# Performance work log

Hardware: AMD Instinct MI355X
Metric: run time of the kernel (lower is better)

Reference implementation:

```python
import jax, jax.numpy as jnp
import numpy as np

B, T = 256, 2048
K_LABELS = 50
K2 = K_LABELS + 2  # includes START (K) and STOP (K+1) tags
NEG_INF = -10000.0


def setup_inputs() -> dict:
    key = jax.random.key(0)
    k1, k2, k3, k4 = jax.random.split(key, 4)
    emissions = jax.random.normal(k1, (B, T, K2), dtype=jnp.float32)
    transitions = jax.random.normal(k2, (K2, K2), dtype=jnp.float32)
    lengths = jax.random.randint(k3, (B,), 1, T + 1, dtype=jnp.int64)
    labels = jax.random.randint(k4, (B, T), 0, K_LABELS, dtype=jnp.int64)
    return {"emissions": emissions, "transitions": transitions,
            "lengths": lengths, "labels": labels}


def _forward_algo(emissions, transitions, lengths):
    b, t, k2 = emissions.shape
    start_tag, stop_tag = k2 - 2, k2 - 1
    init = jnp.full((k2,), NEG_INF, emissions.dtype).at[start_tag].set(0.0)
    alpha0 = jnp.broadcast_to(init, (b, k2))  # [B, K2]

    def step(alpha, emit):
        # tag_var[b, next, prev] = emit[b, next] + trans[next, prev] + alpha[b, prev]
        tag_var = emit[:, :, None] + transitions[None, :, :] + alpha[:, None, :]
        new_alpha = jax.nn.logsumexp(tag_var, axis=2)  # [B, K2]
        return new_alpha, new_alpha

    _, alphas = jax.lax.scan(step, alpha0, jnp.swapaxes(emissions, 0, 1))
    all_alphas = jnp.concatenate([alpha0[None], alphas], axis=0)  # [T+1, B, K2]
    fv = all_alphas[lengths, jnp.arange(b)]  # alpha at each sequence's final step
    terminal = fv + transitions[stop_tag][None, :]
    return jax.nn.logsumexp(terminal, axis=1)  # [B]


def _score_label(emissions, transitions, lengths, labels):
    b, t, k2 = emissions.shape
    start_tag, stop_tag = k2 - 2, k2 - 1
    start_col = jnp.full((b, 1), start_tag, labels.dtype)
    stop_col = jnp.full((b, 1), stop_tag, labels.dtype)
    pad_start = jnp.concatenate([start_col, labels], axis=1)  # [B, T+1]
    pad_stop = jnp.concatenate([labels, stop_col], axis=1)    # [B, T+1]
    pos = jnp.arange(t + 1)
    pad_stop = jnp.where(pos[None, :] >= lengths[:, None], stop_tag, pad_stop)
    # transition score over positions 0..length (inclusive)
    trans_mask = pos[None, :] <= lengths[:, None]
    trans_sc = jnp.where(trans_mask, transitions[pad_stop, pad_start], 0.0).sum(axis=1)
    # emission score over positions 0..length-1
    emit_mask = jnp.arange(t)[None, :] < lengths[:, None]
    emit_vals = jnp.take_along_axis(emissions, labels[..., None], axis=-1)[..., 0]
    emit_sc = jnp.where(emit_mask, emit_vals, 0.0).sum(axis=1)
    return trans_sc + emit_sc  # [B]


def reference(emissions, transitions, lengths, labels):
    forward_score = _forward_algo(emissions, transitions, lengths)
    gold_score = _score_label(emissions, transitions, lengths, labels)
    return jnp.mean(forward_score - gold_score)
```

## Files before the change

### kernel.cpp

```cpp
#include <hip/hip_runtime.h>


#define B_    256
#define T_    2048
#define K2_   52
#define LOG2E_ 1.4426950408889634f
#define LN2_   0.6931471805599453f

__device__ __forceinline__ int imin(int a, int b) { return a < b ? a : b; }
__device__ __forceinline__ int imax(int a, int b) { return a > b ? a : b; }

#define FORALL52(F) \
  F(0) F(1) F(2) F(3) F(4) F(5) F(6) F(7) F(8) F(9) F(10) F(11) F(12) F(13) \
  F(14) F(15) F(16) F(17) F(18) F(19) F(20) F(21) F(22) F(23) F(24) F(25) \
  F(26) F(27) F(28) F(29) F(30) F(31) F(32) F(33) F(34) F(35) F(36) F(37) \
  F(38) F(39) F(40) F(41) F(42) F(43) F(44) F(45) F(46) F(47) F(48) F(49) \
  F(50) F(51)

#define DECLM_F(i) float M_##i; { float _t = tr[n * K2_ + i] * LOG2E_; \
  asm("v_exp_f32 %0, %1\n\ts_nop 1" : "=v"(M_##i) : "v"(_t)); }
#define DECLM_B(i) float M_##i; { float _t = tr[i * K2_ + n] * LOG2E_; \
  asm("v_exp_f32 %0, %1\n\ts_nop 1" : "=v"(M_##i) : "v"(_t)); }

#define ACCQ(Q, i0,i1,i2,i3) \
  _a0 = fmaf(M_##i0, (Q).x, _a0); \
  _a1 = fmaf(M_##i1, (Q).y, _a1); \
  _a2 = fmaf(M_##i2, (Q).z, _a2); \
  _a3 = fmaf(M_##i3, (Q).w, _a3);

#define ACC_ALL \
  ACCQ(_q0 , 0, 1, 2, 3)  ACCQ(_q1 , 4, 5, 6, 7)  ACCQ(_q2 , 8, 9,10,11) \
  ACCQ(_q3 ,12,13,14,15)  ACCQ(_q4 ,16,17,18,19)  ACCQ(_q5 ,20,21,22,23) \
  ACCQ(_q6 ,24,25,26,27)  ACCQ(_q7 ,28,29,30,31)  ACCQ(_q8 ,32,33,34,35) \
  ACCQ(_q9 ,36,37,38,39)  ACCQ(_q10,40,41,42,43)  ACCQ(_q11,44,45,46,47) \
  ACCQ(_qc ,48,49,50,51)

#define MATVEC_F(OUTY, RENORMV) \
    const float4* _g4 = (const float4*)sh; \
    float4 _qc  = _g4[12]; \
    float4 _q0  = _g4[0],  _q1  = _g4[1],  _q2  = _g4[2],  _q3  = _g4[3]; \
    float4 _q4  = _g4[4],  _q5  = _g4[5],  _q6  = _g4[6],  _q7  = _g4[7]; \
    float4 _q8  = _g4[8],  _q9  = _g4[9],  _q10 = _g4[10], _q11 = _g4[11]; \
    float RENORMV = _qc.z; (void)RENORMV; \
    float _a0 = 0.0f, _a1 = 0.0f, _a2 = 0.0f, _a3 = 0.0f; \
    ACC_ALL \
    float OUTY = (_a0 + _a1) + (_a2 + _a3);

#define MATVEC_B(OUTY, RENORMV) \
    const float4* _g4 = (const float4*)sh; \
    float4 _q0  = _g4[0]; \
    float4 _q1  = _g4[1],  _q2  = _g4[2],  _q3  = _g4[3],  _q4  = _g4[4]; \
    float4 _q5  = _g4[5],  _q6  = _g4[6],  _q7  = _g4[7],  _q8  = _g4[8]; \
    float4 _q9  = _g4[9],  _q10 = _g4[10], _q11 = _g4[11], _qc  = _g4[12]; \
    float RENORMV = _q0.x; (void)RENORMV; \
    float _a0 = 0.0f, _a1 = 0.0f, _a2 = 0.0f, _a3 = 0.0f; \
    ACC_ALL \
    float OUTY = (_a0 + _a1) + (_a2 + _a3);

#define FSTEP_R(EV, NEWIDX) do {                                \
    float _ne  = emb[(size_t)(NEWIDX) * K2_ + n];               \
    MATVEC_F(_y, _m)                                            \
    float _inv = __builtin_amdgcn_rcpf(_m);                     \
    C += __builtin_amdgcn_logf(_m);                             \
    float _E = __builtin_amdgcn_exp2f((EV) * LOG2E_);           \
    vv = _y * (_inv * _E);                                      \
    sh[lane] = vv;                                              \
    EV = _ne;                                                   \
  } while (0)
#define FSTEP_N(EV, NEWIDX) do {                                \
    float _ne  = emb[(size_t)(NEWIDX) * K2_ + n];               \
    MATVEC_F(_y, _mu)                                           \
    float _E = __builtin_amdgcn_exp2f((EV) * LOG2E_);           \
    vv = _y * _E;                                               \
    sh[lane] = vv;                                              \
    EV = _ne;                                                   \
  } while (0)

#define BSTEP_R(EV, NEWIDX) do {                                \
    float _ne  = emb[(size_t)(NEWIDX) * K2_ + n];               \
    MATVEC_B(_y, _m)                                            \
    float _inv = __builtin_amdgcn_rcpf(_m);                     \
    C += __builtin_amdgcn_logf(_m);                             \
    vv = _y * _inv;                                             \
    float _E = __builtin_amdgcn_exp2f((EV) * LOG2E_);           \
    sh[lane] = vv * _E;                                         \
    EV = _ne;                                                   \
  } while (0)
#define BSTEP_N(EV, NEWIDX) do {                                \
    float _ne  = emb[(size_t)(NEWIDX) * K2_ + n];               \
    MATVEC_B(_y, _mu)                                           \
    vv = _y;                                                    \
    float _E = __builtin_amdgcn_exp2f((EV) * LOG2E_);           \
    sh[lane] = vv * _E;                                         \
    EV = _ne;                                                   \
  } while (0)

__launch_bounds__(128, 1)
__global__ void crf_fwd_kernel(const float* __restrict__ em,
                               const float* __restrict__ tr,
                               const int*  __restrict__ len,
                               const int*  __restrict__ lab,
                               float* __restrict__ per_b)
{
  const int b    = blockIdx.x;
  const int tid  = threadIdx.x;
  const int wave = tid >> 6;
  const int lane = tid & 63;
  const int n    = (lane < K2_) ? lane : (K2_ - 1);
  const int L    = len[b];
  const int h    = L >> 1;
  const float* emb = em + (size_t)b * (T_ * K2_);

  __shared__ __align__(16) float sV[2][64];
  __shared__ float sCb[1];
  __shared__ float sG[2];

  float* sh = sV[wave];
  float vv, C = 0.0f;

  if (wave == 0) {
    FORALL52(DECLM_F)
    vv = (lane == 50) ? 1.0f : 0.0f;
    sh[lane] = vv;
    float e0 = emb[0 * K2_ + n];
    float e1 = emb[1 * K2_ + n];
    float e2 = emb[2 * K2_ + n];
    float e3 = emb[3 * K2_ + n];
    int t = 0;
    for (; t + 4 <= h; t += 4) {
      int i4 = imin(t + 4, T_ - 1), i5 = imin(t + 5, T_ - 1);
      int i6 = imin(t + 6, T_ - 1), i7 = imin(t + 7, T_ - 1);
      FSTEP_R(e0, i4);
      FSTEP_N(e1, i5);
      FSTEP_N(e2, i6);
      FSTEP_N(e3, i7);
    }
    int rem = h - t;
    if (rem > 0) FSTEP_R(e0, T_ - 1);
    if (rem > 1) FSTEP_N(e1, T_ - 1);
    if (rem > 2) FSTEP_N(e2, T_ - 1);
  } else {
    FORALL52(DECLM_B)
    vv = __builtin_amdgcn_exp2f(tr[(K2_ - 1) * K2_ + n] * LOG2E_);
    int cnt = L - h;
    float e0 = emb[(size_t)(L - 1) * K2_ + n];
    float eA = emb[(size_t)imax(L - 2, 0) * K2_ + n];
    float eB = emb[(size_t)imax(L - 3, 0) * K2_ + n];
    float eC = emb[(size_t)imax(L - 4, 0) * K2_ + n];
    float eD = emb[(size_t)imax(L - 5, 0) * K2_ + n];
    sh[lane] = vv * __builtin_amdgcn_exp2f(e0 * LOG2E_);
    int s = 0;
    for (; s + 4 <= cnt; s += 4) {
      int j4 = imax(L - 6 - s, 0), j5 = imax(L - 7 - s, 0);
      int j6 = imax(L - 8 - s, 0), j7 = imax(L - 9 - s, 0);
      BSTEP_R(eA, j4);
      BSTEP_N(eB, j5);
      BSTEP_N(eC, j6);
      BSTEP_N(eD, j7);
    }
    int rem = cnt - s;
    if (rem > 0) BSTEP_R(eA, 0);
    if (rem > 1) BSTEP_N(eB, 0);
    if (rem > 2) BSTEP_N(eC, 0);

    sh[lane] = vv;
    if (lane == 0) sCb[0] = C;
  }

  float gold = 0.0f;
  const int* labb = lab + b * T_;
  for (int tt = tid; tt < L; tt += 128) {
    int l1 = labb[tt];
    int l0 = (tt == 0) ? 50 : labb[tt - 1];
    gold += emb[(size_t)tt * K2_ + l1] + tr[l1 * K2_ + l0];
  }
  if (tid == 0) gold += tr[(K2_ - 1) * K2_ + labb[L - 1]];
#pragma unroll
  for (int off = 32; off >= 1; off >>= 1)
    gold += __shfl_xor(gold, off, 64);
  if (lane == 0) sG[wave] = gold;

  __syncthreads();

  if (wave == 0) {
    float x = (lane < K2_) ? vv * sV[1][lane] : 0.0f;
#pragma unroll
    for (int off = 32; off >= 1; off >>= 1)
      x += __shfl_xor(x, off, 64);
    float fwd = (C + sCb[0] + __builtin_amdgcn_logf(x)) * LN2_;
    if (lane == 0) per_b[b] = fwd - (sG[0] + sG[1]);
  }
}

__global__ void reduce_mean_kernel(const float* __restrict__ per_b,
                                   float* __restrict__ out)
{
  const int tid = threadIdx.x;
  float v = per_b[tid];
#pragma unroll
  for (int off = 32; off >= 1; off >>= 1) v += __shfl_xor(v, off, 64);
  __shared__ float s[4];
  if ((tid & 63) == 0) s[tid >> 6] = v;
  __syncthreads();
  if (tid == 0) out[0] = ((s[0] + s[1]) + (s[2] + s[3])) * (1.0f / (float)B_);
}

extern "C" void kernel_launch(void* const* d_in, const int* in_sizes, int n_in,
                              void* d_out, int out_size, void* d_ws, size_t ws_size,
                              hipStream_t stream) {
  const float* em  = (const float*)d_in[0];
  const float* tr  = (const float*)d_in[1];
  const int*   len = (const int*)d_in[2];
  const int*   lab = (const int*)d_in[3];
  float* out = (float*)d_out;
  float* ws  = (float*)d_ws;

  crf_fwd_kernel<<<B_, 128, 0, stream>>>(em, tr, len, lab, ws);
  reduce_mean_kernel<<<1, 256, 0, stream>>>(ws, out);
}
```

Baseline: 395.4 us.

## Interleave forward and backward recursions in a single wave per sequence

Instead of two waves each running one half-chain (forward alpha and backward beta), one 64-lane wave now holds both transition matrices in registers and interleaves forward and backward steps. The two independent dependency chains can hide each other's LDS and transcendental latency, and the block barrier and shared-memory merge go away. Shared-memory reads in the matvec are also split into two batches of eight float4 loads that reuse registers. In exchange each wave needs about 104 matrix registers plus temporaries, which raises register pressure and risks spills, and the 256 blocks now supply only 256 waves in total.

```diff
diff --git a/kernel.cpp b/kernel.cpp
--- a/kernel.cpp
+++ b/kernel.cpp
@@ -17,44 +17,62 @@
   F(38) F(39) F(40) F(41) F(42) F(43) F(44) F(45) F(46) F(47) F(48) F(49) \
   F(50) F(51)
 
-#define DECLM_F(i) float M_##i; { float _t = tr[n * K2_ + i] * LOG2E_; \
-  asm("v_exp_f32 %0, %1\n\ts_nop 1" : "=v"(M_##i) : "v"(_t)); }
-#define DECLM_B(i) float M_##i; { float _t = tr[i * K2_ + n] * LOG2E_; \
-  asm("v_exp_f32 %0, %1\n\ts_nop 1" : "=v"(M_##i) : "v"(_t)); }
-
-#define ACCQ(Q, i0,i1,i2,i3) \
-  _a0 = fmaf(M_##i0, (Q).x, _a0); \
-  _a1 = fmaf(M_##i1, (Q).y, _a1); \
-  _a2 = fmaf(M_##i2, (Q).z, _a2); \
-  _a3 = fmaf(M_##i3, (Q).w, _a3);
-
-#define ACC_ALL \
-  ACCQ(_q0 , 0, 1, 2, 3)  ACCQ(_q1 , 4, 5, 6, 7)  ACCQ(_q2 , 8, 9,10,11) \
-  ACCQ(_q3 ,12,13,14,15)  ACCQ(_q4 ,16,17,18,19)  ACCQ(_q5 ,20,21,22,23) \
-  ACCQ(_q6 ,24,25,26,27)  ACCQ(_q7 ,28,29,30,31)  ACCQ(_q8 ,32,33,34,35) \
-  ACCQ(_q9 ,36,37,38,39)  ACCQ(_q10,40,41,42,43)  ACCQ(_q11,44,45,46,47) \
-  ACCQ(_qc ,48,49,50,51)
+#define DECLMF(i) float MF_##i; { float _t = tr[n * K2_ + i] * LOG2E_; \
+  asm("v_exp_f32 %0, %1\n\ts_nop 1" : "=v"(MF_##i) : "v"(_t)); }
+#define DECLMB(i) float MB_##i; { float _t = tr[i * K2_ + n] * LOG2E_; \
+  asm("v_exp_f32 %0, %1\n\ts_nop 1" : "=v"(MB_##i) : "v"(_t)); }
+
+#define ACCQF(Q, i0,i1,i2,i3) \
+  _a0 = fmaf(MF_##i0, (Q).x, _a0); \
+  _a1 = fmaf(MF_##i1, (Q).y, _a1); \
+  _a2 = fmaf(MF_##i2, (Q).z, _a2); \
+  _a3 = fmaf(MF_##i3, (Q).w, _a3);
+#define ACCQB(Q, i0,i1,i2,i3) \
+  _a0 = fmaf(MB_##i0, (Q).x, _a0); \
+  _a1 = fmaf(MB_##i1, (Q).y, _a1); \
+  _a2 = fmaf(MB_##i2, (Q).z, _a2); \
+  _a3 = fmaf(MB_##i3, (Q).w, _a3);
 
 #define MATVEC_F(OUTY, RENORMV) \
-    const float4* _g4 = (const float4*)sh; \
-    float4 _qc  = _g4[12]; \
-    float4 _q0  = _g4[0],  _q1  = _g4[1],  _q2  = _g4[2],  _q3  = _g4[3]; \
-    float4 _q4  = _g4[4],  _q5  = _g4[5],  _q6  = _g4[6],  _q7  = _g4[7]; \
-    float4 _q8  = _g4[8],  _q9  = _g4[9],  _q10 = _g4[10], _q11 = _g4[11]; \
-    float RENORMV = _qc.z; (void)RENORMV; \
+    const float4* _g4 = (const float4*)sF; \
+    float4 _r0 = _g4[12], _r1 = _g4[0], _r2 = _g4[1], _r3 = _g4[2]; \
+    float4 _r4 = _g4[3],  _r5 = _g4[4], _r6 = _g4[5], _r7 = _g4[6]; \
+    float RENORMV = _r0.z; (void)RENORMV; \
     float _a0 = 0.0f, _a1 = 0.0f, _a2 = 0.0f, _a3 = 0.0f; \
-    ACC_ALL \
+    ACCQF(_r0,48,49,50,51)  _r0 = _g4[7]; \
+    ACCQF(_r1, 0, 1, 2, 3)  _r1 = _g4[8]; \
+    ACCQF(_r2, 4, 5, 6, 7)  _r2 = _g4[9]; \
+    ACCQF(_r3, 8, 9,10,11)  _r3 = _g4[10]; \
+    ACCQF(_r4,12,13,14,15)  _r4 = _g4[11]; \
+    ACCQF(_r5,16,17,18,19) \
+    ACCQF(_r6,20,21,22,23) \
+    ACCQF(_r7,24,25,26,27) \
+    ACCQF(_r0,28,29,30,31) \
+    ACCQF(_r1,32,33,34,35) \
+    ACCQF(_r2,36,37,38,39) \
+    ACCQF(_r3,40,41,42,43) \
+    ACCQF(_r4,44,45,46,47) \
     float OUTY = (_a0 + _a1) + (_a2 + _a3);
 
 #define MATVEC_B(OUTY, RENORMV) \
-    const float4* _g4 = (const float4*)sh; \
-    float4 _q0  = _g4[0]; \
-    float4 _q1  = _g4[1],  _q2  = _g4[2],  _q3  = _g4[3],  _q4  = _g4[4]; \
-    float4 _q5  = _g4[5],  _q6  = _g4[6],  _q7  = _g4[7],  _q8  = _g4[8]; \
-    float4 _q9  = _g4[9],  _q10 = _g4[10], _q11 = _g4[11], _qc  = _g4[12]; \
-    float RENORMV = _q0.x; (void)RENORMV; \
+    const float4* _g4 = (const float4*)sB; \
+    float4 _r0 = _g4[0], _r1 = _g4[1], _r2 = _g4[2], _r3 = _g4[3]; \
+    float4 _r4 = _g4[4], _r5 = _g4[5], _r6 = _g4[6], _r7 = _g4[7]; \
+    float RENORMV = _r0.x; (void)RENORMV; \
     float _a0 = 0.0f, _a1 = 0.0f, _a2 = 0.0f, _a3 = 0.0f; \
-    ACC_ALL \
+    ACCQB(_r0, 0, 1, 2, 3)  _r0 = _g4[8]; \
+    ACCQB(_r1, 4, 5, 6, 7)  _r1 = _g4[9]; \
+    ACCQB(_r2, 8, 9,10,11)  _r2 = _g4[10]; \
+    ACCQB(_r3,12,13,14,15)  _r3 = _g4[11]; \
+    ACCQB(_r4,16,17,18,19)  _r4 = _g4[12]; \
+    ACCQB(_r5,20,21,22,23) \
+    ACCQB(_r6,24,25,26,27) \
+    ACCQB(_r7,28,29,30,31) \
+    ACCQB(_r0,32,33,34,35) \
+    ACCQB(_r1,36,37,38,39) \
+    ACCQB(_r2,40,41,42,43) \
+    ACCQB(_r3,44,45,46,47) \
+    ACCQB(_r4,48,49,50,51) \
     float OUTY = (_a0 + _a1) + (_a2 + _a3);
 
 #define FSTEP_R(EV, NEWIDX) do {                                \
@@ -63,16 +81,16 @@
     float _inv = __builtin_amdgcn_rcpf(_m);                     \
     C += __builtin_amdgcn_logf(_m);                             \
     float _E = __builtin_amdgcn_exp2f((EV) * LOG2E_);           \
-    vv = _y * (_inv * _E);                                      \
-    sh[lane] = vv;                                              \
+    vf = _y * (_inv * _E);                                      \
+    sF[lane] = vf;                                              \
     EV = _ne;                                                   \
   } while (0)
 #define FSTEP_N(EV, NEWIDX) do {                                \
     float _ne  = emb[(size_t)(NEWIDX) * K2_ + n];               \
     MATVEC_F(_y, _mu)                                           \
     float _E = __builtin_amdgcn_exp2f((EV) * LOG2E_);           \
-    vv = _y * _E;                                               \
-    sh[lane] = vv;                                              \
+    vf = _y * _E;                                               \
+    sF[lane] = vf;                                              \
     EV = _ne;                                                   \
   } while (0)
 
@@ -81,21 +99,21 @@
     MATVEC_B(_y, _m)                                            \
     float _inv = __builtin_amdgcn_rcpf(_m);                     \
     C += __builtin_amdgcn_logf(_m);                             \
-    vv = _y * _inv;                                             \
-    float _E = __builtin_amdgcn_exp2f((EV) * LOG2E_);           \
-    sh[lane] = vv * _E;                                         \
+    vb = _y * _inv;                                             \
+    float _E = __builtin_amdgcn_exp2f((EV) * LOG2E_);           \
+    sB[lane] = vb * _E;                                         \
     EV = _ne;                                                   \
   } while (0)
 #define BSTEP_N(EV, NEWIDX) do {                                \
     float _ne  = emb[(size_t)(NEWIDX) * K2_ + n];               \
     MATVEC_B(_y, _mu)                                           \
-    vv = _y;                                                    \
-    float _E = __builtin_amdgcn_exp2f((EV) * LOG2E_);           \
-    sh[lane] = vv * _E;                                         \
-    EV = _ne;                                                   \
-  } while (0)
-
-__launch_bounds__(128, 1)
+    vb = _y;                                                    \
+    float _E = __builtin_amdgcn_exp2f((EV) * LOG2E_);           \
+    sB[lane] = vb * _E;                                         \
+    EV = _ne;                                                   \
+  } while (0)
+
+__launch_bounds__(64, 1)
 __global__ void crf_fwd_kernel(const float* __restrict__ em,
                                const float* __restrict__ tr,
                                const int*  __restrict__ len,
@@ -103,93 +121,76 @@
                                float* __restrict__ per_b)
 {
   const int b    = blockIdx.x;
-  const int tid  = threadIdx.x;
-  const int wave = tid >> 6;
-  const int lane = tid & 63;
+  const int lane = threadIdx.x & 63;
   const int n    = (lane < K2_) ? lane : (K2_ - 1);
   const int L    = len[b];
   const int h    = L >> 1;
+  const int cnt  = L - h;
   const float* emb = em + (size_t)b * (T_ * K2_);
 
-  __shared__ __align__(16) float sV[2][64];
-  __shared__ float sCb[1];
-  __shared__ float sG[2];
-
-  float* sh = sV[wave];
-  float vv, C = 0.0f;
-
-  if (wave == 0) {
-    FORALL52(DECLM_F)
-    vv = (lane == 50) ? 1.0f : 0.0f;
-    sh[lane] = vv;
-    float e0 = emb[0 * K2_ + n];
-    float e1 = emb[1 * K2_ + n];
-    float e2 = emb[2 * K2_ + n];
-    float e3 = emb[3 * K2_ + n];
-    int t = 0;
-    for (; t + 4 <= h; t += 4) {
-      int i4 = imin(t + 4, T_ - 1), i5 = imin(t + 5, T_ - 1);
-      int i6 = imin(t + 6, T_ - 1), i7 = imin(t + 7, T_ - 1);
-      FSTEP_R(e0, i4);
-      FSTEP_N(e1, i5);
-      FSTEP_N(e2, i6);
-      FSTEP_N(e3, i7);
-    }
-    int rem = h - t;
-    if (rem > 0) FSTEP_R(e0, T_ - 1);
-    if (rem > 1) FSTEP_N(e1, T_ - 1);
-    if (rem > 2) FSTEP_N(e2, T_ - 1);
-  } else {
-    FORALL52(DECLM_B)
-    vv = __builtin_amdgcn_exp2f(tr[(K2_ - 1) * K2_ + n] * LOG2E_);
-    int cnt = L - h;
-    float e0 = emb[(size_t)(L - 1) * K2_ + n];
-    float eA = emb[(size_t)imax(L - 2, 0) * K2_ + n];
-    float eB = emb[(size_t)imax(L - 3, 0) * K2_ + n];
-    float eC = emb[(size_t)imax(L - 4, 0) * K2_ + n];
-    float eD = emb[(size_t)imax(L - 5, 0) * K2_ + n];
-    sh[lane] = vv * __builtin_amdgcn_exp2f(e0 * LOG2E_);
-    int s = 0;
-    for (; s + 4 <= cnt; s += 4) {
-      int j4 = imax(L - 6 - s, 0), j5 = imax(L - 7 - s, 0);
-      int j6 = imax(L - 8 - s, 0), j7 = imax(L - 9 - s, 0);
-      BSTEP_R(eA, j4);
-      BSTEP_N(eB, j5);
-      BSTEP_N(eC, j6);
-      BSTEP_N(eD, j7);
-    }
-    int rem = cnt - s;
-    if (rem > 0) BSTEP_R(eA, 0);
-    if (rem > 1) BSTEP_N(eB, 0);
-    if (rem > 2) BSTEP_N(eC, 0);
-
-    sh[lane] = vv;
-    if (lane == 0) sCb[0] = C;
+  __shared__ __align__(16) float sF[64];
+  __shared__ __align__(16) float sB[64];
+
+  float C = 0.0f;
+
+  FORALL52(DECLMF)
+  FORALL52(DECLMB)
+
+  float vf = (lane == 50) ? 1.0f : 0.0f;
+  sF[lane] = vf;
+  float f0 = emb[0 * K2_ + n];
+  float f1 = emb[1 * K2_ + n];
+  float f2 = emb[2 * K2_ + n];
+  float f3 = emb[3 * K2_ + n];
+
+  float vb = __builtin_amdgcn_exp2f(tr[(K2_ - 1) * K2_ + n] * LOG2E_);
+  float e0 = emb[(size_t)(L - 1) * K2_ + n];
+  float bA = emb[(size_t)imax(L - 2, 0) * K2_ + n];
+  float bB = emb[(size_t)imax(L - 3, 0) * K2_ + n];
+  float bC = emb[(size_t)imax(L - 4, 0) * K2_ + n];
+  float bD = emb[(size_t)imax(L - 5, 0) * K2_ + n];
+  sB[lane] = vb * __builtin_amdgcn_exp2f(e0 * LOG2E_);
+
+  int t = 0;
+  for (; t + 4 <= h; t += 4) {
+    int i4 = imin(t + 4, T_ - 1), i5 = imin(t + 5, T_ - 1);
+    int i6 = imin(t + 6, T_ - 1), i7 = imin(t + 7, T_ - 1);
+    int j4 = imax(L - 6 - t, 0), j5 = imax(L - 7 - t, 0);
+    int j6 = imax(L - 8 - t, 0), j7 = imax(L - 9 - t, 0);
+    FSTEP_R(f0, i4);  BSTEP_R(bA, j4);
+    FSTEP_N(f1, i5);  BSTEP_N(bB, j5);
+    FSTEP_N(f2, i6);  BSTEP_N(bC, j6);
+    FSTEP_N(f3, i7);  BSTEP_N(bD, j7);
+  }
+  int rem = h - t;
+  if (rem > 0) { FSTEP_R(f0, T_ - 1); BSTEP_R(bA, 0); }
+  if (rem > 1) { FSTEP_N(f1, T_ - 1); BSTEP_N(bB, 0); }
+  if (rem > 2) { FSTEP_N(f2, T_ - 1); BSTEP_N(bC, 0); }
+  if (cnt > h) {
+    if      (rem == 0) BSTEP_R(bA, 0);
+    else if (rem == 1) BSTEP_N(bB, 0);
+    else if (rem == 2) BSTEP_N(bC, 0);
+    else               BSTEP_N(bD, 0);
   }
 
   float gold = 0.0f;
   const int* labb = lab + b * T_;
-  for (int tt = tid; tt < L; tt += 128) {
+  for (int tt = lane; tt < L; tt += 64) {
     int l1 = labb[tt];
     int l0 = (tt == 0) ? 50 : labb[tt - 1];
     gold += emb[(size_t)tt * K2_ + l1] + tr[l1 * K2_ + l0];
   }
-  if (tid == 0) gold += tr[(K2_ - 1) * K2_ + labb[L - 1]];
+  if (lane == 0) gold += tr[(K2_ - 1) * K2_ + labb[L - 1]];
 #pragma unroll
   for (int off = 32; off >= 1; off >>= 1)
     gold += __shfl_xor(gold, off, 64);
-  if (lane == 0) sG[wave] = gold;
-
-  __syncthreads();
-
-  if (wave == 0) {
-    float x = (lane < K2_) ? vv * sV[1][lane] : 0.0f;
+
+  float x = (lane < K2_) ? vf * vb : 0.0f;
 #pragma unroll
-    for (int off = 32; off >= 1; off >>= 1)
-      x += __shfl_xor(x, off, 64);
-    float fwd = (C + sCb[0] + __builtin_amdgcn_logf(x)) * LN2_;
-    if (lane == 0) per_b[b] = fwd - (sG[0] + sG[1]);
-  }
+  for (int off = 32; off >= 1; off >>= 1)
+    x += __shfl_xor(x, off, 64);
+  if (lane == 0)
+    per_b[b] = (C + __builtin_amdgcn_logf(x)) * LN2_ - gold;
 }
 
 __global__ void reduce_mean_kernel(const float* __restrict__ per_b,
@@ -215,6 +216,6 @@
   float* out = (float*)d_out;
   float* ws  = (float*)d_ws;
 
-  crf_fwd_kernel<<<B_, 128, 0, stream>>>(em, tr, len, lab, ws);
+  crf_fwd_kernel<<<B_, 64, 0, stream>>>(em, tr, len, lab, ws);
   reduce_mean_kernel<<<1, 256, 0, stream>>>(ws, out);
 }
```

After: 595.1 us. +50.5%, slower.
